# Optimization experiments

Measured on AMD Instinct MI355X. Metric: run time of the kernel, lower is better.

## Reference

```python
import jax, jax.numpy as jnp
import numpy as np

IN, OUT, E, R = 2048, 2048, 8, 8

def setup_inputs() -> dict:
    key = jax.random.key(0)
    ks = jax.random.split(key, 8)
    B, S = 4, 2048
    x = jax.random.normal(ks[0], (B, S, IN), dtype=jnp.float32)
    routing_weights = jax.random.uniform(ks[1], (B, E), dtype=jnp.float32)
    W = jax.random.normal(ks[2], (OUT, IN), dtype=jnp.float32) / np.sqrt(IN).astype(np.float32)
    b = jax.random.normal(ks[3], (OUT,), dtype=jnp.float32) * 0.01
    lora_A_s = jax.random.normal(ks[4], (IN, R), dtype=jnp.float32) / np.sqrt(IN).astype(np.float32)
    lora_B_s = jax.random.normal(ks[5], (R, OUT), dtype=jnp.float32) * 0.01
    lora_A_e = jax.random.normal(ks[6], (E, IN, R), dtype=jnp.float32) / np.sqrt(IN).astype(np.float32)
    lora_B_e = jax.random.normal(ks[7], (E, R, OUT), dtype=jnp.float32) * 0.01
    return {"x": x, "routing_weights": routing_weights, "W": W, "b": b,
            "lora_A_s": lora_A_s, "lora_B_s": lora_B_s,
            "lora_A_e": lora_A_e, "lora_B_e": lora_B_e}

def reference(x, routing_weights, W, b, lora_A_s, lora_B_s, lora_A_e, lora_B_e):
    # base linear: [B,S,IN] @ [IN,OUT] + [OUT]
    base_out = jnp.einsum('bsi,oi->bso', x, W) + b
    # shared low-rank path
    shared_out = (x @ lora_A_s) @ lora_B_s
    # all experts batched: t[b,s,e,r] = x @ A_e[e]; weighted reduce over experts
    t = jnp.einsum('bsi,eir->bser', x, lora_A_e)          # [B,S,E,R]
    expert_out = jnp.einsum('bser,ero,be->bso', t, lora_B_e, routing_weights)
    return base_out + shared_out + expert_out
```

## Files before the change

kernel.cpp:

```cpp
#include <hip/hip_runtime.h>
#include <hip/hip_bf16.h>

#define IN_DIM 2048
#define OUT_DIM 2048
#define NE 8
#define M_TOT 8192
#define RANK_PAD 128
#define K_EXT 2176
#define NKT 34

typedef short short8 __attribute__((ext_vector_type(8)));
typedef float floatx4 __attribute__((ext_vector_type(4)));
typedef unsigned short us;

__device__ __forceinline__ us f2bf(float f) {
    union { float f; unsigned u; } v; v.f = f;
    unsigned r = v.u + 0x7FFFu + ((v.u >> 16) & 1u);
    return (us)(r >> 16);
}

__device__ __forceinline__ void gld_lds16(const void* g, void* l) {
    __builtin_amdgcn_global_load_lds(
        (const __attribute__((address_space(1))) void*)g,
        (__attribute__((address_space(3))) void*)l, 16, 0, 0);
}


__device__ __forceinline__ void stage_half(int h, const us* __restrict__ A,
                                           const us* __restrict__ B,
                                           int m0, int n0, int tid, char* smem) {
    int tau = h >> 2, part = h & 3;
    const us* g = (part & 1) ? (B + (size_t)n0 * K_EXT) : (A + (size_t)m0 * K_EXT);
    int kbase = tau * 64 + (part >> 1) * 32;
    char* lb = smem + (tau & 1) * 65536 + part * 16384 + (tid >> 6) * 1024;
#pragma unroll
    for (int j = 0; j < 2; ++j) {
        int q = j * 512 + tid;
        int r = q >> 2, ps = q & 3;
        const us* src = g + (size_t)r * K_EXT + kbase + ((ps ^ ((r >> 1) & 3)) * 8);
        gld_lds16(src, lb + j * 8192);
    }
}

__device__ __forceinline__ void mfma_quad(floatx4 (&acc)[8][4], const short8 (&af)[4],
                                          const short8 (&bf)[4], int mq) {
#pragma unroll
    for (int i = 0; i < 4; ++i)
#pragma unroll
        for (int ni = 0; ni < 4; ++ni)
            acc[mq * 4 + i][ni] =
                __builtin_amdgcn_mfma_f32_16x16x32_bf16(af[i], bf[ni], acc[mq * 4 + i][ni], 0, 0, 0);
}

template <int SMASK, int VMN>
__device__ __forceinline__ void ktile(int t, char* smem, const us* __restrict__ A,
                                      const us* __restrict__ B, int m0, int n0, int tid,
                                      int abyte0, int bbyte0, floatx4 (&acc)[8][4]) {
    const char* sm = smem + (t & 1) * 65536;
    const int sbase = 4 * t + 7;
    short8 af[4], bf[4];

#pragma unroll
    for (int ni = 0; ni < 4; ++ni) bf[ni] = *(const short8*)(sm + bbyte0 + ni * 1024);
#pragma unroll
    for (int i = 0; i < 4; ++i) af[i] = *(const short8*)(sm + abyte0 + i * 1024);
    if (SMASK & 1) stage_half(sbase + 0, A, B, m0, n0, tid, smem);
    __builtin_amdgcn_s_barrier();
    asm volatile("s_waitcnt lgkmcnt(0)" ::: "memory");
    __builtin_amdgcn_s_setprio(1);
    mfma_quad(acc, af, bf, 0);
    __builtin_amdgcn_s_setprio(0);
    __builtin_amdgcn_s_barrier();

#pragma unroll
    for (int i = 0; i < 4; ++i) af[i] = *(const short8*)(sm + abyte0 + (4 + i) * 1024);
    if (SMASK & 2) stage_half(sbase + 1, A, B, m0, n0, tid, smem);
    __builtin_amdgcn_s_barrier();
    asm volatile("s_waitcnt lgkmcnt(0)" ::: "memory");
    __builtin_amdgcn_s_setprio(1);
    mfma_quad(acc, af, bf, 1);
    __builtin_amdgcn_s_setprio(0);
    __builtin_amdgcn_s_barrier();

#pragma unroll
    for (int ni = 0; ni < 4; ++ni) bf[ni] = *(const short8*)(sm + 32768 + bbyte0 + ni * 1024);
#pragma unroll
    for (int i = 0; i < 4; ++i) af[i] = *(const short8*)(sm + 32768 + abyte0 + (4 + i) * 1024);
    if (SMASK & 4) stage_half(sbase + 2, A, B, m0, n0, tid, smem);
    __builtin_amdgcn_s_barrier();
    asm volatile("s_waitcnt lgkmcnt(0)" ::: "memory");
    __builtin_amdgcn_s_setprio(1);
    mfma_quad(acc, af, bf, 1);
    __builtin_amdgcn_s_setprio(0);
    __builtin_amdgcn_s_barrier();

#pragma unroll
    for (int i = 0; i < 4; ++i) af[i] = *(const short8*)(sm + 32768 + abyte0 + i * 1024);
    if (SMASK & 8) stage_half(sbase + 3, A, B, m0, n0, tid, smem);
    __builtin_amdgcn_s_barrier();
    asm volatile("s_waitcnt lgkmcnt(0)" ::: "memory");
    __builtin_amdgcn_s_setprio(1);
    mfma_quad(acc, af, bf, 0);
    __builtin_amdgcn_s_setprio(0);
    if (VMN == 6) asm volatile("s_waitcnt vmcnt(6)" ::: "memory");
    else if (VMN == 0) asm volatile("s_waitcnt vmcnt(0)" ::: "memory");
    __builtin_amdgcn_s_barrier();
}

__global__ __launch_bounds__(512) void main_gemm8(const us* __restrict__ A,
                                                  const us* __restrict__ B,
                                                  const float* __restrict__ bias,
                                                  float* __restrict__ out) {
    extern __shared__ char smem[];
    int tid = threadIdx.x;
    int lane = tid & 63, w = tid >> 6;
    int wm = w >> 2, wn = w & 3;
    int rlo = lane & 15, kq = lane >> 4;
    int m0 = blockIdx.y * 256, n0 = blockIdx.x * 256;
    int swz = (kq ^ ((rlo >> 1) & 3)) * 16;
    int abyte0 = (wm * 128 + rlo) * 64 + swz;
    int bbyte0 = 16384 + (wn * 64 + rlo) * 64 + swz;

    floatx4 acc[8][4];
#pragma unroll
    for (int mi = 0; mi < 8; ++mi)
#pragma unroll
        for (int ni = 0; ni < 4; ++ni) acc[mi][ni] = (floatx4)0.f;

#pragma unroll
    for (int h = 0; h < 7; ++h) stage_half(h, A, B, m0, n0, tid, smem);
    asm volatile("s_waitcnt vmcnt(6)" ::: "memory");
    __builtin_amdgcn_s_barrier();

    for (int t = 0; t < 32; ++t)
        ktile<0xF, 6>(t, smem, A, B, m0, n0, tid, abyte0, bbyte0, acc);
    ktile<0x1, 0>(32, smem, A, B, m0, n0, tid, abyte0, bbyte0, acc);
    ktile<0x0, -1>(33, smem, A, B, m0, n0, tid, abyte0, bbyte0, acc);

    float bb[4];
#pragma unroll
    for (int ni = 0; ni < 4; ++ni) bb[ni] = bias[n0 + wn * 64 + ni * 16 + rlo];
#pragma unroll
    for (int mi = 0; mi < 8; ++mi) {
        int row = m0 + wm * 128 + mi * 16 + kq * 4;
#pragma unroll
        for (int ni = 0; ni < 4; ++ni) {
            int col = n0 + wn * 64 + ni * 16 + rlo;
#pragma unroll
            for (int r = 0; r < 4; ++r)
                out[(size_t)(row + r) * OUT_DIM + col] = acc[mi][ni][r] + bb[ni];
        }
    }
}

__global__ void prep_w(const float* __restrict__ W, const float* __restrict__ Bs,
                       const float* __restrict__ Be, us* __restrict__ Bext) {
    int n = blockIdx.x;
    int t = threadIdx.x;
    const float4* src = (const float4*)(W + (size_t)n * IN_DIM + t * 8);
    float4 v0 = src[0], v1 = src[1];
    short8 o;
    o[0] = (short)f2bf(v0.x); o[1] = (short)f2bf(v0.y); o[2] = (short)f2bf(v0.z); o[3] = (short)f2bf(v0.w);
    o[4] = (short)f2bf(v1.x); o[5] = (short)f2bf(v1.y); o[6] = (short)f2bf(v1.z); o[7] = (short)f2bf(v1.w);
    *(short8*)(Bext + (size_t)n * K_EXT + t * 8) = o;
    if (t < RANK_PAD) {
        float v = 0.f;
        if (t < 8)       v = Bs[(size_t)t * OUT_DIM + n];
        else if (t < 72) v = Be[(size_t)(t - 8) * OUT_DIM + n];
        Bext[(size_t)n * K_EXT + IN_DIM + t] = f2bf(v);
    }
}

__global__ void prep_acat(const float* __restrict__ As, const float* __restrict__ Ae,
                          us* __restrict__ AcatT) {
    int kp = blockIdx.x;
    int i0 = threadIdx.x * 8;
    short8 o;
#pragma unroll
    for (int j = 0; j < 8; ++j) {
        int i = i0 + j;
        float v = 0.f;
        if (kp < 8)       v = As[(size_t)i * 8 + kp];
        else if (kp < 72) v = Ae[(size_t)((kp - 8) >> 3) * IN_DIM * 8 + (size_t)i * 8 + ((kp - 8) & 7)];
        o[j] = (short)f2bf(v);
    }
    *(short8*)(AcatT + (size_t)kp * IN_DIM + i0) = o;
}

__global__ __launch_bounds__(256) void tgemm_fused(const float* __restrict__ x,
                                                   us* __restrict__ Aext,
                                                   const us* __restrict__ AcatT,
                                                   const float* __restrict__ routing) {
    __shared__ floatx4 red[4][64][6];
    int tid = threadIdx.x;
    int lane = tid & 63, w = tid >> 6;
    int rlo = lane & 15, kq = lane >> 4;
    int mbase = blockIdx.x * 16;

    floatx4 acc[6];
#pragma unroll
    for (int ni = 0; ni < 6; ++ni) acc[ni] = (floatx4)0.f;

    const float* xrow = x + (size_t)(mbase + rlo) * IN_DIM + w * 512 + kq * 8;
    us* arow = Aext + (size_t)(mbase + rlo) * K_EXT + w * 512 + kq * 8;
    const us* bbase = AcatT + (size_t)rlo * IN_DIM + w * 512 + kq * 8;

#pragma unroll 4
    for (int kt = 0; kt < 16; ++kt) {
        int k0 = kt * 32;
        float4 v0 = *(const float4*)(xrow + k0);
        float4 v1 = *(const float4*)(xrow + k0 + 4);
        short8 a;
        a[0] = (short)f2bf(v0.x); a[1] = (short)f2bf(v0.y); a[2] = (short)f2bf(v0.z); a[3] = (short)f2bf(v0.w);
        a[4] = (short)f2bf(v1.x); a[5] = (short)f2bf(v1.y); a[6] = (short)f2bf(v1.z); a[7] = (short)f2bf(v1.w);
        *(short8*)(arow + k0) = a;
#pragma unroll
        for (int ni = 0; ni < 6; ++ni) {
            short8 b = *(const short8*)(bbase + (size_t)(ni * 16) * IN_DIM + k0);
            acc[ni] = __builtin_amdgcn_mfma_f32_16x16x32_bf16(a, b, acc[ni], 0, 0, 0);
        }
    }

#pragma unroll
    for (int ni = 0; ni < 6; ++ni) red[w][lane][ni] = acc[ni];
    __syncthreads();
    if (w == 0) {
#pragma unroll
        for (int ni = 0; ni < 6; ++ni) {
            floatx4 s = red[0][lane][ni];
#pragma unroll
            for (int ww = 1; ww < 4; ++ww) s += red[ww][lane][ni];
            int col = ni * 16 + rlo;
#pragma unroll
            for (int r = 0; r < 4; ++r) {
                int row = mbase + kq * 4 + r;
                float fac = (col < 8) ? 1.f
                          : (col < 72 ? routing[(row >> 11) * NE + ((col - 8) >> 3)] : 0.f);
                Aext[(size_t)row * K_EXT + IN_DIM + col] = f2bf(s[r] * fac);
            }
        }
#pragma unroll
        for (int c = 0; c < 2; ++c) {
            int col = 96 + c * 16 + rlo;
#pragma unroll
            for (int r = 0; r < 4; ++r)
                Aext[(size_t)(mbase + kq * 4 + r) * K_EXT + IN_DIM + col] = 0;
        }
    }
}

extern "C" void kernel_launch(void* const* d_in, const int* in_sizes, int n_in,
                              void* d_out, int out_size, void* d_ws, size_t ws_size,
                              hipStream_t stream) {
    const float* x   = (const float*)d_in[0];
    const float* rw  = (const float*)d_in[1];
    const float* W   = (const float*)d_in[2];
    const float* bv  = (const float*)d_in[3];
    const float* As  = (const float*)d_in[4];
    const float* Bs  = (const float*)d_in[5];
    const float* Ae  = (const float*)d_in[6];
    const float* Be  = (const float*)d_in[7];
    float* out = (float*)d_out;

    size_t offA = 0;
    size_t offB = offA + (size_t)M_TOT * K_EXT * sizeof(us);
    size_t offC = offB + (size_t)OUT_DIM * K_EXT * sizeof(us);
    size_t need = offC + (size_t)96 * IN_DIM * sizeof(us);
    if (ws_size < need) return;

    us* Aext  = (us*)((char*)d_ws + offA);
    us* Bext  = (us*)((char*)d_ws + offB);
    us* AcatT = (us*)((char*)d_ws + offC);

    hipFuncSetAttribute((const void*)main_gemm8,
                        hipFuncAttributeMaxDynamicSharedMemorySize, 131072);

    prep_acat<<<96, 256, 0, stream>>>(As, Ae, AcatT);
    prep_w<<<OUT_DIM, 256, 0, stream>>>(W, Bs, Be, Bext);
    tgemm_fused<<<M_TOT / 16, 256, 0, stream>>>(x, Aext, AcatT, rw);
    main_gemm8<<<dim3(OUT_DIM / 256, M_TOT / 256), 512, 131072, stream>>>(Aext, Bext, bv, out);
}
```

Before: 121.8 us.

## Software-pipeline LDS fragment reads across subtiles and remap blocks for cache locality

Reworks the main GEMM k-loop so that LDS fragment loads for the next MFMA quad are issued before the current quad runs. Partial lgkmcnt waits and sched_barriers replace the full waits and double barriers per quad, cutting barrier count per k-tile. Global-to-LDS staging now uses precomputed per-thread pointers with a changed vmcnt schedule. The launch becomes a 1D grid with a swizzled block-to-tile mapping intended to improve L2 reuse across concurrently running blocks. Tighter synchronisation raises the risk of LDS read/write races if the wait counts are wrong.

```diff
diff --git a/kernel.cpp b/kernel.cpp
--- a/kernel.cpp
+++ b/kernel.cpp
@@ -26,20 +26,9 @@
 }
 
 
-__device__ __forceinline__ void stage_half(int h, const us* __restrict__ A,
-                                           const us* __restrict__ B,
-                                           int m0, int n0, int tid, char* smem) {
-    int tau = h >> 2, part = h & 3;
-    const us* g = (part & 1) ? (B + (size_t)n0 * K_EXT) : (A + (size_t)m0 * K_EXT);
-    int kbase = tau * 64 + (part >> 1) * 32;
-    char* lb = smem + (tau & 1) * 65536 + part * 16384 + (tid >> 6) * 1024;
-#pragma unroll
-    for (int j = 0; j < 2; ++j) {
-        int q = j * 512 + tid;
-        int r = q >> 2, ps = q & 3;
-        const us* src = g + (size_t)r * K_EXT + kbase + ((ps ^ ((r >> 1) & 3)) * 8);
-        gld_lds16(src, lb + j * 8192);
-    }
+__device__ __forceinline__ void stage2(const us* src, char* lds) {
+    gld_lds16(src, lds);
+    gld_lds16(src + 128 * K_EXT, lds + 8192);
 }
 
 __device__ __forceinline__ void mfma_quad(floatx4 (&acc)[8][4], const short8 (&af)[4],
@@ -52,58 +41,64 @@
                 __builtin_amdgcn_mfma_f32_16x16x32_bf16(af[i], bf[ni], acc[mq * 4 + i][ni], 0, 0, 0);
 }
 
-template <int SMASK, int VMN>
-__device__ __forceinline__ void ktile(int t, char* smem, const us* __restrict__ A,
-                                      const us* __restrict__ B, int m0, int n0, int tid,
-                                      int abyte0, int bbyte0, floatx4 (&acc)[8][4]) {
-    const char* sm = smem + (t & 1) * 65536;
-    const int sbase = 4 * t + 7;
-    short8 af[4], bf[4];
-
-#pragma unroll
-    for (int ni = 0; ni < 4; ++ni) bf[ni] = *(const short8*)(sm + bbyte0 + ni * 1024);
-#pragma unroll
-    for (int i = 0; i < 4; ++i) af[i] = *(const short8*)(sm + abyte0 + i * 1024);
-    if (SMASK & 1) stage_half(sbase + 0, A, B, m0, n0, tid, smem);
-    __builtin_amdgcn_s_barrier();
-    asm volatile("s_waitcnt lgkmcnt(0)" ::: "memory");
+template <int SM, int VM0, int VM2, bool RD3>
+__device__ __forceinline__ void ktile(
+    const us* __restrict__ pA, const us* __restrict__ pB, int k1, int k2,
+    const char* smC, const char* smN, char* lwC, char* lwN,
+    int ab, int bb,
+    short8 (&afA)[4], short8 (&afB)[4], short8 (&bfA)[4], short8 (&bfB)[4],
+    floatx4 (&acc)[8][4])
+{
+#pragma unroll
+    for (int i = 0; i < 4; ++i) afB[i] = *(const short8*)(smC + ab + (4 + i) * 1024);
+    asm volatile("s_waitcnt lgkmcnt(4)" ::: "memory");
+    __builtin_amdgcn_sched_barrier(0);
     __builtin_amdgcn_s_setprio(1);
-    mfma_quad(acc, af, bf, 0);
+    mfma_quad(acc, afA, bfA, 0);
     __builtin_amdgcn_s_setprio(0);
-    __builtin_amdgcn_s_barrier();
-
-#pragma unroll
-    for (int i = 0; i < 4; ++i) af[i] = *(const short8*)(sm + abyte0 + (4 + i) * 1024);
-    if (SMASK & 2) stage_half(sbase + 1, A, B, m0, n0, tid, smem);
-    __builtin_amdgcn_s_barrier();
-    asm volatile("s_waitcnt lgkmcnt(0)" ::: "memory");
+    if (SM & 1) stage2(pA + k1 + 32, lwN + 32768);
+    if (VM0 == 8)      asm volatile("s_waitcnt vmcnt(8)" ::: "memory");
+    else if (VM0 == 0) asm volatile("s_waitcnt vmcnt(0)" ::: "memory");
+    __builtin_amdgcn_s_barrier();
+
+#pragma unroll
+    for (int i = 0; i < 4; ++i) afA[i] = *(const short8*)(smC + 32768 + ab + (4 + i) * 1024);
+#pragma unroll
+    for (int i = 0; i < 4; ++i) bfB[i] = *(const short8*)(smC + 32768 + bb + i * 1024);
+    asm volatile("s_waitcnt lgkmcnt(8)" ::: "memory");
+    __builtin_amdgcn_sched_barrier(0);
     __builtin_amdgcn_s_setprio(1);
-    mfma_quad(acc, af, bf, 1);
+    mfma_quad(acc, afB, bfA, 1);
     __builtin_amdgcn_s_setprio(0);
-    __builtin_amdgcn_s_barrier();
-
-#pragma unroll
-    for (int ni = 0; ni < 4; ++ni) bf[ni] = *(const short8*)(sm + 32768 + bbyte0 + ni * 1024);
-#pragma unroll
-    for (int i = 0; i < 4; ++i) af[i] = *(const short8*)(sm + 32768 + abyte0 + (4 + i) * 1024);
-    if (SMASK & 4) stage_half(sbase + 2, A, B, m0, n0, tid, smem);
-    __builtin_amdgcn_s_barrier();
-    asm volatile("s_waitcnt lgkmcnt(0)" ::: "memory");
+    if (SM & 2) stage2(pB + k2, lwC + 16384);
+    __builtin_amdgcn_s_barrier();
+
+#pragma unroll
+    for (int i = 0; i < 4; ++i) afB[i] = *(const short8*)(smC + 32768 + ab + i * 1024);
+    asm volatile("s_waitcnt lgkmcnt(4)" ::: "memory");
+    __builtin_amdgcn_sched_barrier(0);
     __builtin_amdgcn_s_setprio(1);
-    mfma_quad(acc, af, bf, 1);
+    mfma_quad(acc, afA, bfB, 1);
     __builtin_amdgcn_s_setprio(0);
-    __builtin_amdgcn_s_barrier();
-
-#pragma unroll
-    for (int i = 0; i < 4; ++i) af[i] = *(const short8*)(sm + 32768 + abyte0 + i * 1024);
-    if (SMASK & 8) stage_half(sbase + 3, A, B, m0, n0, tid, smem);
-    __builtin_amdgcn_s_barrier();
-    asm volatile("s_waitcnt lgkmcnt(0)" ::: "memory");
+    if (SM & 4) stage2(pA + k2, lwC);
+    if (VM2 == 8)      asm volatile("s_waitcnt vmcnt(8)" ::: "memory");
+    else if (VM2 == 4) asm volatile("s_waitcnt vmcnt(4)" ::: "memory");
+    __builtin_amdgcn_s_barrier();
+
+    if (RD3) {
+#pragma unroll
+        for (int i = 0; i < 4; ++i) afA[i] = *(const short8*)(smN + ab + i * 1024);
+#pragma unroll
+        for (int i = 0; i < 4; ++i) bfA[i] = *(const short8*)(smN + bb + i * 1024);
+        asm volatile("s_waitcnt lgkmcnt(8)" ::: "memory");
+    } else {
+        asm volatile("s_waitcnt lgkmcnt(0)" ::: "memory");
+    }
+    __builtin_amdgcn_sched_barrier(0);
     __builtin_amdgcn_s_setprio(1);
-    mfma_quad(acc, af, bf, 0);
+    mfma_quad(acc, afB, bfB, 0);
     __builtin_amdgcn_s_setprio(0);
-    if (VMN == 6) asm volatile("s_waitcnt vmcnt(6)" ::: "memory");
-    else if (VMN == 0) asm volatile("s_waitcnt vmcnt(0)" ::: "memory");
+    if (SM & 8) stage2(pB + k2 + 32, lwC + 49152);
     __builtin_amdgcn_s_barrier();
 }
 
@@ -116,10 +111,24 @@
     int lane = tid & 63, w = tid >> 6;
     int wm = w >> 2, wn = w & 3;
     int rlo = lane & 15, kq = lane >> 4;
-    int m0 = blockIdx.y * 256, n0 = blockIdx.x * 256;
+
+    int b = blockIdx.x;
+    int bs = (b & 7) * 32 + (b >> 3);
+    int m0 = (bs >> 3) * 256, n0 = (bs & 7) * 256;
+
     int swz = (kq ^ ((rlo >> 1) & 3)) * 16;
-    int abyte0 = (wm * 128 + rlo) * 64 + swz;
-    int bbyte0 = 16384 + (wn * 64 + rlo) * 64 + swz;
+    int ab = (wm * 128 + rlo) * 64 + swz;
+    int bb = 16384 + (wn * 64 + rlo) * 64 + swz;
+
+    int r0 = tid >> 2;
+    int ps = tid & 3;
+    int ssw = (ps ^ ((r0 >> 1) & 3)) * 8;
+    const us* pA = A + (size_t)(m0 + r0) * K_EXT + ssw;
+    const us* pB = B + (size_t)(n0 + r0) * K_EXT + ssw;
+    char* lw0 = smem + w * 1024;
+    char* lw1 = lw0 + 65536;
+    const char* sm0 = smem;
+    const char* sm1 = smem + 65536;
 
     floatx4 acc[8][4];
 #pragma unroll
@@ -127,19 +136,37 @@
 #pragma unroll
         for (int ni = 0; ni < 4; ++ni) acc[mi][ni] = (floatx4)0.f;
 
-#pragma unroll
-    for (int h = 0; h < 7; ++h) stage_half(h, A, B, m0, n0, tid, smem);
-    asm volatile("s_waitcnt vmcnt(6)" ::: "memory");
-    __builtin_amdgcn_s_barrier();
-
-    for (int t = 0; t < 32; ++t)
-        ktile<0xF, 6>(t, smem, A, B, m0, n0, tid, abyte0, bbyte0, acc);
-    ktile<0x1, 0>(32, smem, A, B, m0, n0, tid, abyte0, bbyte0, acc);
-    ktile<0x0, -1>(33, smem, A, B, m0, n0, tid, abyte0, bbyte0, acc);
-
-    float bb[4];
-#pragma unroll
-    for (int ni = 0; ni < 4; ++ni) bb[ni] = bias[n0 + wn * 64 + ni * 16 + rlo];
+    stage2(pA,      lw0);
+    stage2(pB,      lw0 + 16384);
+    stage2(pA + 32, lw0 + 32768);
+    stage2(pB + 32, lw0 + 49152);
+    stage2(pA + 64, lw1);
+    stage2(pB + 64, lw1 + 16384);
+    stage2(pB + 96, lw1 + 49152);
+    asm volatile("s_waitcnt vmcnt(10)" ::: "memory");
+    __builtin_amdgcn_s_barrier();
+
+    short8 afA[4], afB[4], bfA[4], bfB[4];
+#pragma unroll
+    for (int i = 0; i < 4; ++i) afA[i] = *(const short8*)(sm0 + ab + i * 1024);
+#pragma unroll
+    for (int i = 0; i < 4; ++i) bfA[i] = *(const short8*)(sm0 + bb + i * 1024);
+
+    for (int tt = 0; tt < 16; ++tt) {
+        int t0 = tt * 2;
+        ktile<0xF, 8, 8, true>(pA, pB, (t0 + 1) * 64, (t0 + 2) * 64,
+                               sm0, sm1, lw0, lw1, ab, bb, afA, afB, bfA, bfB, acc);
+        ktile<0xF, 8, 8, true>(pA, pB, (t0 + 2) * 64, (t0 + 3) * 64,
+                               sm1, sm0, lw1, lw0, ab, bb, afA, afB, bfA, bfB, acc);
+    }
+    ktile<0x1, 8, 4, true>(pA, pB, 33 * 64, 34 * 64,
+                           sm0, sm1, lw0, lw1, ab, bb, afA, afB, bfA, bfB, acc);
+    ktile<0x0, 0, -1, false>(pA, pB, 0, 0,
+                             sm1, sm0, lw1, lw0, ab, bb, afA, afB, bfA, bfB, acc);
+
+    float bbias[4];
+#pragma unroll
+    for (int ni = 0; ni < 4; ++ni) bbias[ni] = bias[n0 + wn * 64 + ni * 16 + rlo];
 #pragma unroll
     for (int mi = 0; mi < 8; ++mi) {
         int row = m0 + wm * 128 + mi * 16 + kq * 4;
@@ -148,7 +175,7 @@
             int col = n0 + wn * 64 + ni * 16 + rlo;
 #pragma unroll
             for (int r = 0; r < 4; ++r)
-                out[(size_t)(row + r) * OUT_DIM + col] = acc[mi][ni][r] + bb[ni];
+                out[(size_t)(row + r) * OUT_DIM + col] = acc[mi][ni][r] + bbias[ni];
         }
     }
 }
@@ -216,8 +243,8 @@
         *(short8*)(arow + k0) = a;
 #pragma unroll
         for (int ni = 0; ni < 6; ++ni) {
-            short8 b = *(const short8*)(bbase + (size_t)(ni * 16) * IN_DIM + k0);
-            acc[ni] = __builtin_amdgcn_mfma_f32_16x16x32_bf16(a, b, acc[ni], 0, 0, 0);
+            short8 bfr = *(const short8*)(bbase + (size_t)(ni * 16) * IN_DIM + k0);
+            acc[ni] = __builtin_amdgcn_mfma_f32_16x16x32_bf16(a, bfr, acc[ni], 0, 0, 0);
         }
     }
 
@@ -278,5 +305,5 @@
     prep_acat<<<96, 256, 0, stream>>>(As, Ae, AcatT);
     prep_w<<<OUT_DIM, 256, 0, stream>>>(W, Bs, Be, Bext);
     tgemm_fused<<<M_TOT / 16, 256, 0, stream>>>(x, Aext, AcatT, rw);
-    main_gemm8<<<dim3(OUT_DIM / 256, M_TOT / 256), 512, 131072, stream>>>(Aext, Bext, bv, out);
-}
+    main_gemm8<<<256, 512, 131072, stream>>>(Aext, Bext, bv, out);
+}
```

New measurement: 117.4 us. -3.6%, faster.
